# Kernel tuning notes

Hardware: AMD Instinct MI355X
Metric: run time of the kernel (lower is better)

## Reference

```python
import jax, jax.numpy as jnp
import numpy as np

B, N, F_NUM, H_NUM = 2, 8192, 64, 64


def _linear_params(key, fan_in, fan_out, bias=True):
    k1, k2 = jax.random.split(key)
    bound = 1.0 / np.sqrt(fan_in)
    W = jax.random.uniform(k1, (fan_in, fan_out), minval=-bound, maxval=bound, dtype=jnp.float32)
    if bias:
        b = jax.random.uniform(k2, (fan_out,), minval=-bound, maxval=bound, dtype=jnp.float32)
        return W, b
    return W


def setup_inputs() -> dict:
    key = jax.random.key(0)
    ks = jax.random.split(key, 12)
    Wk, bk = _linear_params(ks[0], F_NUM, H_NUM)
    Wa, ba = _linear_params(ks[1], H_NUM, F_NUM)
    Wq = _linear_params(ks[2], H_NUM, H_NUM, bias=False)
    Wks = _linear_params(ks[3], H_NUM, H_NUM, bias=False)
    Wv = _linear_params(ks[4], H_NUM, H_NUM, bias=False)
    Wp1, bp1 = _linear_params(ks[5], 4, H_NUM)
    Wp2, bp2 = _linear_params(ks[6], H_NUM, H_NUM)
    Wt1, bt1 = _linear_params(ks[7], H_NUM, H_NUM)
    Wt2, bt2 = _linear_params(ks[8], H_NUM, H_NUM)
    xyzp = jax.random.normal(ks[9], (B, N, 4), dtype=jnp.float32)
    features = jax.random.normal(ks[10], (B, N, F_NUM), dtype=jnp.float32)
    return dict(xyzp=xyzp, features=features, Wk=Wk, bk=bk, Wq=Wq, Wks=Wks, Wv=Wv,
                Wp1=Wp1, bp1=bp1, Wp2=Wp2, bp2=bp2, Wt1=Wt1, bt1=bt1, Wt2=Wt2, bt2=bt2,
                Wa=Wa, ba=ba, k_nearest=16)


def _knn_idx(xyz, K):
    sq = jnp.sum(xyz * xyz, axis=-1)                      # [B,N]
    d = sq[:, :, None] + sq[:, None, :] - 2.0 * jnp.einsum('bnd,bmd->bnm', xyz, xyz)
    _, idx = jax.lax.top_k(-d, K)                         # [B,N,K] nearest (incl. self)
    return idx


def _knn_gather(x, idx):
    # x: [B,N,C], idx: [B,N,K] -> [B,N,K,C]
    return jax.vmap(lambda xb, ib: xb[ib])(x, idx)


def reference(xyzp, features, Wk, bk, Wq, Wks, Wv, Wp1, bp1, Wp2, bp2,
              Wt1, bt1, Wt2, bt2, Wa, ba, k_nearest):
    xyz = xyzp[:, :, :3]
    idx = _knn_idx(xyz, k_nearest)                        # [B,N,K]
    # positional encoding MLP on relative xyzp
    rel = xyzp[:, :, None, :] - _knn_gather(xyzp, idx)    # [B,N,K,4]
    pos_enc = jax.nn.relu(rel @ Wp1 + bp1) @ Wp2 + bp2    # [B,N,K,H]
    x = features @ Wk + bk                                # [B,N,H]
    q = x @ Wq                                            # [B,N,H]
    k = _knn_gather(x @ Wks, idx)                         # [B,N,K,H]
    v = _knn_gather(x @ Wv, idx)                          # [B,N,K,H]
    a_in = q[:, :, None, :] - k + pos_enc                 # [B,N,K,H]
    attn = jax.nn.relu(a_in @ Wt1 + bt1) @ Wt2 + bt2      # [B,N,K,H]
    attn = jax.nn.softmax(attn / np.sqrt(H_NUM).astype(np.float32), axis=-2)
    res = jnp.einsum('bnkh,bnkh->bnh', attn, v + pos_enc) # per-channel weighted sum over K
    return res @ Wa + ba + features
```

## Files before the change

### kernel.cpp

```cpp
#include <hip/hip_runtime.h>

#define NPTS 8192
#define HDIM 64
#define KNN 16
#define LOG2E 1.4426950408889634f

typedef __attribute__((ext_vector_type(8))) short bf8_t;
typedef __attribute__((ext_vector_type(4))) float f4_t;
#define MFMA16(a, b, c) __builtin_amdgcn_mfma_f32_16x16x32_bf16(a, b, c, 0, 0, 0)

__device__ __forceinline__ float fast_exp(float x) {
    float y = x * LOG2E;
    float r;
    asm volatile("v_exp_f32 %0, %1\n\ts_nop 1" : "=v"(r) : "v"(y));
    return r;
}
__device__ __forceinline__ unsigned short f2b(float x) {
    unsigned v = __float_as_uint(x);
    return (unsigned short)((v + 0x7FFFu + ((v >> 16) & 1u)) >> 16);
}

#define OFF_QW   0u
#define OFF_KW   (4u << 20)
#define OFF_VW   (8u << 20)
#define OFF_FRAG (12u << 20)
#define OFF_KNN  ((12u << 20) + 32768u)

__global__ void prefrag_kernel(const float* __restrict__ Wp2,
                               const float* __restrict__ Wt1,
                               const float* __restrict__ Wt2,
                               unsigned short* __restrict__ dst)
{
    int i = blockIdx.x * 256 + threadIdx.x;
    if (i >= 3 * 4096) return;
    int st = i >> 12, e = i & 4095;
    const float* W = (st == 0) ? Wp2 : (st == 1) ? Wt1 : Wt2;
    int k = e >> 6, n = e & 63;
    int s = k >> 5, quad = (k >> 3) & 3, j = k & 7;
    int t = n >> 4, l = quad * 16 + (n & 15);
    dst[st * 4096 + (s * 4 + t) * 512 + l * 8 + j] = f2b(W[e]);
}

__global__ __launch_bounds__(1024) void proj_kernel(
    const float* __restrict__ feat,
    const float* __restrict__ Wk, const float* __restrict__ bk,
    const float* __restrict__ Wq, const float* __restrict__ Wks,
    const float* __restrict__ Wv,
    float* __restrict__ qw, float* __restrict__ kw, float* __restrict__ vw)
{
    __shared__ __align__(16) float4 sW[4][1024];
    int tid = threadIdx.x;
    sW[0][tid] = ((const float4*)Wk)[tid];
    sW[1][tid] = ((const float4*)Wq)[tid];
    sW[2][tid] = ((const float4*)Wks)[tid];
    sW[3][tid] = ((const float4*)Wv)[tid];
    __syncthreads();
    const float* sWk  = (const float*)sW[0];
    const float* sWq  = (const float*)sW[1];
    const float* sWks = (const float*)sW[2];
    const float* sWv  = (const float*)sW[3];

    int w = tid >> 6, lane = tid & 63;
    int p = blockIdx.x * 16 + w;
    float f = feat[(size_t)p * HDIM + lane];
    float x = bk[lane];
    #pragma unroll 8
    for (int c = 0; c < 64; ++c) x += __shfl(f, c) * sWk[c * 64 + lane];
    float q = 0.f, k = 0.f, v = 0.f;
    #pragma unroll 8
    for (int c = 0; c < 64; ++c) {
        float xc = __shfl(x, c);
        q += xc * sWq[c * 64 + lane];
        k += xc * sWks[c * 64 + lane];
        v += xc * sWv[c * 64 + lane];
    }
    qw[(size_t)p * HDIM + lane] = q;
    kw[(size_t)p * HDIM + lane] = k;
    vw[(size_t)p * HDIM + lane] = v;
}

__global__ __launch_bounds__(256) void knn4_kernel(
    const float* __restrict__ xyzp, int* __restrict__ knnIdx)
{
    int w = threadIdx.x >> 6, lane = threadIdx.x & 63;
    int wid = blockIdx.x * 4 + w;
    int pbase = wid * 4;
    int b = pbase >> 13;
    int nbase = pbase & (NPTS - 1);
    const float4* xb4 = (const float4*)xyzp + (size_t)b * NPTS;

    float qx[4], qy[4], qz[4], qs[4];
    #pragma unroll
    for (int qi = 0; qi < 4; ++qi) {
        float4 s = xb4[nbase + qi];
        qx[qi] = s.x; qy[qi] = s.y; qz[qi] = s.z;
        qs[qi] = s.x * s.x + s.y * s.y + s.z * s.z;
    }

    float dh[4][4]; int ih[4][4];
    #pragma unroll
    for (int qi = 0; qi < 4; ++qi)
        #pragma unroll
        for (int j = 0; j < 4; ++j) { dh[qi][j] = 3.4e38f; ih[qi][j] = 0x7fffffff; }

    for (int t = 0; t < NPTS / 256; ++t) {
        float4 c[4];
        #pragma unroll
        for (int u = 0; u < 4; ++u)
            c[u] = xb4[(t * 4 + u) * 64 + lane];
        #pragma unroll
        for (int u = 0; u < 4; ++u) {
            int m = (t * 4 + u) * 64 + lane;
            float cs = c[u].x * c[u].x + c[u].y * c[u].y + c[u].z * c[u].z;
            #pragma unroll
            for (int qi = 0; qi < 4; ++qi) {
                float d = qs[qi] + cs
                        - 2.0f * (qx[qi] * c[u].x + qy[qi] * c[u].y + qz[qi] * c[u].z);
                if (d < dh[qi][3]) {
                    dh[qi][3] = d; ih[qi][3] = m;
                    #pragma unroll
                    for (int j = 3; j >= 1; --j)
                        if (dh[qi][j] < dh[qi][j - 1]) {
                            float td = dh[qi][j]; dh[qi][j] = dh[qi][j - 1]; dh[qi][j - 1] = td;
                            int ti = ih[qi][j]; ih[qi][j] = ih[qi][j - 1]; ih[qi][j - 1] = ti;
                        }
                }
            }
        }
    }

    #pragma unroll
    for (int qi = 0; qi < 4; ++qi) {
        int mynb = 0, head = 0;
        #pragma unroll 1
        for (int r = 0; r < KNN; ++r) {
            float d = dh[qi][0]; int i = ih[qi][0];
            #pragma unroll
            for (int s = 1; s < 64; s <<= 1) {
                float d2 = __shfl_xor(d, s); int i2 = __shfl_xor(i, s);
                if (d2 < d || (d2 == d && i2 < i)) { d = d2; i = i2; }
            }
            if (lane == r) mynb = i;
            if (ih[qi][0] == i) {
                dh[qi][0] = dh[qi][1]; ih[qi][0] = ih[qi][1];
                dh[qi][1] = dh[qi][2]; ih[qi][1] = ih[qi][2];
                dh[qi][2] = dh[qi][3]; ih[qi][2] = ih[qi][3];
                dh[qi][3] = 3.4e38f; ih[qi][3] = 0x7fffffff;
                ++head;
            }
        }
        if (__any(head >= 4)) {
            float eh[16]; int ei[16];
            #pragma unroll
            for (int j = 0; j < 16; ++j) { eh[j] = 3.4e38f; ei[j] = 0x7fffffff; }
            for (int t = 0; t < NPTS / 64; ++t) {
                int m = t * 64 + lane;
                float4 c4 = xb4[m];
                float cs = c4.x * c4.x + c4.y * c4.y + c4.z * c4.z;
                float d = qs[qi] + cs
                        - 2.0f * (qx[qi] * c4.x + qy[qi] * c4.y + qz[qi] * c4.z);
                if (d < eh[15]) {
                    eh[15] = d; ei[15] = m;
                    #pragma unroll
                    for (int j = 15; j >= 1; --j)
                        if (eh[j] < eh[j - 1]) {
                            float td = eh[j]; eh[j] = eh[j - 1]; eh[j - 1] = td;
                            int ti = ei[j]; ei[j] = ei[j - 1]; ei[j - 1] = ti;
                        }
                }
            }
            #pragma unroll 1
            for (int r = 0; r < KNN; ++r) {
                float d = eh[0]; int i = ei[0];
                #pragma unroll
                for (int s = 1; s < 64; s <<= 1) {
                    float d2 = __shfl_xor(d, s); int i2 = __shfl_xor(i, s);
                    if (d2 < d || (d2 == d && i2 < i)) { d = d2; i = i2; }
                }
                if (lane == r) mynb = i;
                if (ei[0] == i) {
                    #pragma unroll
                    for (int j = 0; j < 15; ++j) { eh[j] = eh[j + 1]; ei[j] = ei[j + 1]; }
                    eh[15] = 3.4e38f; ei[15] = 0x7fffffff;
                }
            }
        }
        mynb = min(max(mynb, 0), NPTS - 1);
        if (lane < KNN) knnIdx[(size_t)(pbase + qi) * KNN + lane] = mynb;
    }
}

__global__ __launch_bounds__(256) void LocalTransformer_80513456931527_kernel(
    const float* __restrict__ xyzp, const float* __restrict__ features,
    const float* __restrict__ Wp1,  const float* __restrict__ bp1,
    const float* __restrict__ bp2,  const float* __restrict__ bt1,
    const float* __restrict__ bt2,
    const float* __restrict__ Wa,   const float* __restrict__ ba,
    const float* __restrict__ qw, const float* __restrict__ kw,
    const float* __restrict__ vw,
    const unsigned short* __restrict__ fragw,
    const int* __restrict__ knnIdx,
    float* __restrict__ out)
{
    __shared__ __align__(16) float sBounce[4][16 * 68 + 4];

    int tid = threadIdx.x, w = tid >> 6, lane = tid & 63;
    int p = blockIdx.x * 4 + w;
    int b = p >> 13;
    float* bb = sBounce[w];

    int quad = lane >> 4, l15 = lane & 15;
    int mynb = knnIdx[(size_t)p * KNN + l15];
    mynb = min(max(mynb, 0), NPTS - 1);
    int nb_a = mynb;
    int nbm[4];
    #pragma unroll
    for (int r = 0; r < 4; ++r) nbm[r] = __shfl(mynb, quad * 4 + r);

    const float4 xq4 = *(const float4*)(xyzp + (size_t)p * 4);
    const float4 xn4 = *(const float4*)(xyzp + ((size_t)b * NPTS + nb_a) * 4);
    float rel0 = xq4.x - xn4.x, rel1 = xq4.y - xn4.y;
    float rel2 = xq4.z - xn4.z, rel3 = xq4.w - xn4.w;

    bf8_t pe1f[2];
    #pragma unroll
    for (int s = 0; s < 2; ++s) {
        int hb = s * 32 + quad * 8;
        float W0[8], W1[8], W2[8], W3[8], Bb[8];
        *(float4*)&W0[0] = *(const float4*)(Wp1 +       hb);
        *(float4*)&W0[4] = *(const float4*)(Wp1 +       hb + 4);
        *(float4*)&W1[0] = *(const float4*)(Wp1 +  64 + hb);
        *(float4*)&W1[4] = *(const float4*)(Wp1 +  64 + hb + 4);
        *(float4*)&W2[0] = *(const float4*)(Wp1 + 128 + hb);
        *(float4*)&W2[4] = *(const float4*)(Wp1 + 128 + hb + 4);
        *(float4*)&W3[0] = *(const float4*)(Wp1 + 192 + hb);
        *(float4*)&W3[4] = *(const float4*)(Wp1 + 192 + hb + 4);
        *(float4*)&Bb[0] = *(const float4*)(bp1 + hb);
        *(float4*)&Bb[4] = *(const float4*)(bp1 + hb + 4);
        #pragma unroll
        for (int j = 0; j < 8; ++j) {
            float a = Bb[j] + rel0 * W0[j] + rel1 * W1[j]
                            + rel2 * W2[j] + rel3 * W3[j];
            pe1f[s][j] = (short)f2b(fmaxf(a, 0.f));
        }
    }

    const bf8_t* BW = (const bf8_t*)fragw;
    f4_t pe2c[4];
    #pragma unroll
    for (int t = 0; t < 4; ++t) {
        f4_t acc = {0.f, 0.f, 0.f, 0.f};
        acc = MFMA16(pe1f[0], BW[0 * 512 + (0 * 4 + t) * 64 + lane], acc);
        acc = MFMA16(pe1f[1], BW[0 * 512 + (1 * 4 + t) * 64 + lane], acc);
        float bias = bp2[t * 16 + l15];
        #pragma unroll
        for (int r = 0; r < 4; ++r) acc[r] += bias;
        pe2c[t] = acc;
    }

    f4_t ainc[4], vpec[4];
    #pragma unroll
    for (int t = 0; t < 4; ++t) {
        float qv = qw[(size_t)p * HDIM + t * 16 + l15];
        #pragma unroll
        for (int r = 0; r < 4; ++r) {
            size_t nbo = ((size_t)b * NPTS + nbm[r]) * HDIM + t * 16 + l15;
            ainc[t][r] = qv - kw[nbo] + pe2c[t][r];
            vpec[t][r] = vw[nbo] + pe2c[t][r];
        }
    }

    #pragma unroll
    for (int t = 0; t < 4; ++t)
        #pragma unroll
        for (int r = 0; r < 4; ++r)
            bb[(quad * 4 + r) * 68 + t * 16 + l15] = ainc[t][r];
    asm volatile("s_waitcnt lgkmcnt(0)" ::: "memory");
    bf8_t af[2];
    #pragma unroll
    for (int s = 0; s < 2; ++s) {
        float tmp[8];
        *(float4*)&tmp[0] = *(const float4*)&bb[l15 * 68 + s * 32 + quad * 8];
        *(float4*)&tmp[4] = *(const float4*)&bb[l15 * 68 + s * 32 + quad * 8 + 4];
        #pragma unroll
        for (int j = 0; j < 8; ++j) af[s][j] = (short)f2b(tmp[j]);
    }

    f4_t t1c[4];
    #pragma unroll
    for (int t = 0; t < 4; ++t) {
        f4_t acc = {0.f, 0.f, 0.f, 0.f};
        acc = MFMA16(af[0], BW[1 * 512 + (0 * 4 + t) * 64 + lane], acc);
        acc = MFMA16(af[1], BW[1 * 512 + (1 * 4 + t) * 64 + lane], acc);
        float bias = bt1[t * 16 + l15];
        #pragma unroll
        for (int r = 0; r < 4; ++r) t1c[t][r] = fmaxf(acc[r] + bias, 0.f);
    }

    asm volatile("s_waitcnt lgkmcnt(0)" ::: "memory");
    #pragma unroll
    for (int t = 0; t < 4; ++t)
        #pragma unroll
        for (int r = 0; r < 4; ++r)
            bb[(quad * 4 + r) * 68 + t * 16 + l15] = t1c[t][r];
    asm volatile("s_waitcnt lgkmcnt(0)" ::: "memory");
    bf8_t tf[2];
    #pragma unroll
    for (int s = 0; s < 2; ++s) {
        float tmp[8];
        *(float4*)&tmp[0] = *(const float4*)&bb[l15 * 68 + s * 32 + quad * 8];
        *(float4*)&tmp[4] = *(const float4*)&bb[l15 * 68 + s * 32 + quad * 8 + 4];
        #pragma unroll
        for (int j = 0; j < 8; ++j) tf[s][j] = (short)f2b(tmp[j]);
    }

    f4_t lgc[4];
    #pragma unroll
    for (int t = 0; t < 4; ++t) {
        f4_t acc = {0.f, 0.f, 0.f, 0.f};
        acc = MFMA16(tf[0], BW[2 * 512 + (0 * 4 + t) * 64 + lane], acc);
        acc = MFMA16(tf[1], BW[2 * 512 + (1 * 4 + t) * 64 + lane], acc);
        float bias = bt2[t * 16 + l15];
        #pragma unroll
        for (int r = 0; r < 4; ++r) lgc[t][r] = (acc[r] + bias) * 0.125f;
    }

    float res[4];
    #pragma unroll
    for (int t = 0; t < 4; ++t) {
        float m0 = fmaxf(fmaxf(lgc[t][0], lgc[t][1]), fmaxf(lgc[t][2], lgc[t][3]));
        m0 = fmaxf(m0, __shfl_xor(m0, 16));
        m0 = fmaxf(m0, __shfl_xor(m0, 32));
        float e0 = fast_exp(lgc[t][0] - m0), e1 = fast_exp(lgc[t][1] - m0);
        float e2 = fast_exp(lgc[t][2] - m0), e3 = fast_exp(lgc[t][3] - m0);
        float sl = e0 + e1 + e2 + e3;
        float rl = e0 * vpec[t][0] + e1 * vpec[t][1]
                 + e2 * vpec[t][2] + e3 * vpec[t][3];
        sl += __shfl_xor(sl, 16); sl += __shfl_xor(sl, 32);
        rl += __shfl_xor(rl, 16); rl += __shfl_xor(rl, 32);
        res[t] = rl / sl;
    }

    float rh = (quad == 0) ? res[0] : (quad == 1) ? res[1]
             : (quad == 2) ? res[2] : res[3];
    float f = features[(size_t)p * HDIM + lane];
    float o = ba[lane];
    #pragma unroll 8
    for (int c = 0; c < 64; ++c) o += __shfl(rh, c) * Wa[c * 64 + lane];
    out[(size_t)p * HDIM + lane] = o + f;
}

extern "C" void kernel_launch(void* const* d_in, const int* in_sizes, int n_in,
                              void* d_out, int out_size, void* d_ws, size_t ws_size,
                              hipStream_t stream)
{
    (void)in_sizes; (void)n_in; (void)out_size; (void)ws_size;
    const float* xyzp     = (const float*)d_in[0];
    const float* features = (const float*)d_in[1];
    const float* Wk  = (const float*)d_in[2];
    const float* bk  = (const float*)d_in[3];
    const float* Wq  = (const float*)d_in[4];
    const float* Wks = (const float*)d_in[5];
    const float* Wv  = (const float*)d_in[6];
    const float* Wp1 = (const float*)d_in[7];
    const float* bp1 = (const float*)d_in[8];
    const float* Wp2 = (const float*)d_in[9];
    const float* bp2 = (const float*)d_in[10];
    const float* Wt1 = (const float*)d_in[11];
    const float* bt1 = (const float*)d_in[12];
    const float* Wt2 = (const float*)d_in[13];
    const float* bt2 = (const float*)d_in[14];
    const float* Wa  = (const float*)d_in[15];
    const float* ba  = (const float*)d_in[16];
    float* out = (float*)d_out;
    char* ws = (char*)d_ws;

    float* qw = (float*)(ws + OFF_QW);
    float* kw = (float*)(ws + OFF_KW);
    float* vw = (float*)(ws + OFF_VW);
    unsigned short* fragw = (unsigned short*)(ws + OFF_FRAG);
    int* knnIdx = (int*)(ws + OFF_KNN);

    prefrag_kernel<<<48, 256, 0, stream>>>(Wp2, Wt1, Wt2, fragw);
    proj_kernel<<<(2 * NPTS) / 16, 1024, 0, stream>>>(
        features, Wk, bk, Wq, Wks, Wv, qw, kw, vw);
    knn4_kernel<<<(2 * NPTS) / 16, 256, 0, stream>>>(xyzp, knnIdx);
    LocalTransformer_80513456931527_kernel<<<(2 * NPTS) / 4, 256, 0, stream>>>(
        xyzp, features, Wp1, bp1, bp2, bt1, bt2, Wa, ba,
        qw, kw, vw, fragw, knnIdx, out);
}
```

Measured before the change: 375.0 us.

## Split rare KNN fallback path into a separate fix-up kernel

Moves the rare full-rescan fallback (used when one lane contributed four or more of a query's 16 neighbours) out of the main KNN kernel into a separate knnfix kernel, driven by per-wave failure flags written to the workspace. The main kernel no longer carries the 16-entry register heap, and launch_bounds(256,4) is added, so register pressure should drop and occupancy rise. The cost is one extra kernel launch, whose waves mostly exit early after reading a flag.

```diff
diff --git a/kernel.cpp b/kernel.cpp
--- a/kernel.cpp
+++ b/kernel.cpp
@@ -25,6 +25,7 @@
 #define OFF_VW   (8u << 20)
 #define OFF_FRAG (12u << 20)
 #define OFF_KNN  ((12u << 20) + 32768u)
+#define OFF_FLAG ((13u << 20) + 32768u)
 
 __global__ void prefrag_kernel(const float* __restrict__ Wp2,
                                const float* __restrict__ Wt1,
@@ -79,8 +80,9 @@
     vw[(size_t)p * HDIM + lane] = v;
 }
 
-__global__ __launch_bounds__(256) void knn4_kernel(
-    const float* __restrict__ xyzp, int* __restrict__ knnIdx)
+__global__ __launch_bounds__(256, 4) void knn4_kernel(
+    const float* __restrict__ xyzp, int* __restrict__ knnIdx,
+    int* __restrict__ flagw)
 {
     int w = threadIdx.x >> 6, lane = threadIdx.x & 63;
     int wid = blockIdx.x * 4 + w;
@@ -129,6 +131,7 @@
         }
     }
 
+    int failmask = 0;
     #pragma unroll
     for (int qi = 0; qi < 4; ++qi) {
         int mynb = 0, head = 0;
@@ -149,40 +152,64 @@
                 ++head;
             }
         }
-        if (__any(head >= 4)) {
-            float eh[16]; int ei[16];
+        if (__any(head >= 4)) failmask |= (1 << qi);
+        mynb = min(max(mynb, 0), NPTS - 1);
+        if (lane < KNN) knnIdx[(size_t)(pbase + qi) * KNN + lane] = mynb;
+    }
+    if (lane == 0) flagw[wid] = failmask;
+}
+
+__global__ __launch_bounds__(256) void knnfix_kernel(
+    const float* __restrict__ xyzp, const int* __restrict__ flagw,
+    int* __restrict__ knnIdx)
+{
+    int w = threadIdx.x >> 6, lane = threadIdx.x & 63;
+    int wid = blockIdx.x * 4 + w;
+    int failmask = flagw[wid];
+    if (failmask == 0) return;
+    int pbase = wid * 4;
+    int b = pbase >> 13;
+    int nbase = pbase & (NPTS - 1);
+    const float4* xb4 = (const float4*)xyzp + (size_t)b * NPTS;
+
+    #pragma unroll 1
+    for (int qi = 0; qi < 4; ++qi) {
+        if (!((failmask >> qi) & 1)) continue;
+        float4 s = xb4[nbase + qi];
+        float qx = s.x, qy = s.y, qz = s.z;
+        float qs = qx * qx + qy * qy + qz * qz;
+        float eh[16]; int ei[16];
+        #pragma unroll
+        for (int j = 0; j < 16; ++j) { eh[j] = 3.4e38f; ei[j] = 0x7fffffff; }
+        for (int t = 0; t < NPTS / 64; ++t) {
+            int m = t * 64 + lane;
+            float4 c4 = xb4[m];
+            float cs = c4.x * c4.x + c4.y * c4.y + c4.z * c4.z;
+            float d = qs + cs - 2.0f * (qx * c4.x + qy * c4.y + qz * c4.z);
+            if (d < eh[15]) {
+                eh[15] = d; ei[15] = m;
+                #pragma unroll
+                for (int j = 15; j >= 1; --j)
+                    if (eh[j] < eh[j - 1]) {
+                        float td = eh[j]; eh[j] = eh[j - 1]; eh[j - 1] = td;
+                        int ti = ei[j]; ei[j] = ei[j - 1]; ei[j - 1] = ti;
+                    }
+            }
+        }
+        int mynb = 0;
+        #pragma unroll 1
+        for (int r = 0; r < KNN; ++r) {
+            float d = eh[0]; int i = ei[0];
             #pragma unroll
-            for (int j = 0; j < 16; ++j) { eh[j] = 3.4e38f; ei[j] = 0x7fffffff; }
-            for (int t = 0; t < NPTS / 64; ++t) {
-                int m = t * 64 + lane;
-                float4 c4 = xb4[m];
-                float cs = c4.x * c4.x + c4.y * c4.y + c4.z * c4.z;
-                float d = qs[qi] + cs
-                        - 2.0f * (qx[qi] * c4.x + qy[qi] * c4.y + qz[qi] * c4.z);
-                if (d < eh[15]) {
-                    eh[15] = d; ei[15] = m;
-                    #pragma unroll
-                    for (int j = 15; j >= 1; --j)
-                        if (eh[j] < eh[j - 1]) {
-                            float td = eh[j]; eh[j] = eh[j - 1]; eh[j - 1] = td;
-                            int ti = ei[j]; ei[j] = ei[j - 1]; ei[j - 1] = ti;
-                        }
-                }
-            }
-            #pragma unroll 1
-            for (int r = 0; r < KNN; ++r) {
-                float d = eh[0]; int i = ei[0];
+            for (int s2 = 1; s2 < 64; s2 <<= 1) {
+                float d2 = __shfl_xor(d, s2); int i2 = __shfl_xor(i, s2);
+                if (d2 < d || (d2 == d && i2 < i)) { d = d2; i = i2; }
+            }
+            if (lane == r) mynb = i;
+            if (ei[0] == i) {
                 #pragma unroll
-                for (int s = 1; s < 64; s <<= 1) {
-                    float d2 = __shfl_xor(d, s); int i2 = __shfl_xor(i, s);
-                    if (d2 < d || (d2 == d && i2 < i)) { d = d2; i = i2; }
-                }
-                if (lane == r) mynb = i;
-                if (ei[0] == i) {
-                    #pragma unroll
-                    for (int j = 0; j < 15; ++j) { eh[j] = eh[j + 1]; ei[j] = ei[j + 1]; }
-                    eh[15] = 3.4e38f; ei[15] = 0x7fffffff;
-                }
+                for (int j = 0; j < 15; ++j) { eh[j] = eh[j + 1]; ei[j] = ei[j + 1]; }
+                eh[15] = 3.4e38f; ei[15] = 0x7fffffff;
             }
         }
         mynb = min(max(mynb, 0), NPTS - 1);
@@ -380,11 +407,13 @@
     float* vw = (float*)(ws + OFF_VW);
     unsigned short* fragw = (unsigned short*)(ws + OFF_FRAG);
     int* knnIdx = (int*)(ws + OFF_KNN);
+    int* flagw  = (int*)(ws + OFF_FLAG);
 
     prefrag_kernel<<<48, 256, 0, stream>>>(Wp2, Wt1, Wt2, fragw);
     proj_kernel<<<(2 * NPTS) / 16, 1024, 0, stream>>>(
         features, Wk, bk, Wq, Wks, Wv, qw, kw, vw);
-    knn4_kernel<<<(2 * NPTS) / 16, 256, 0, stream>>>(xyzp, knnIdx);
+    knn4_kernel<<<(2 * NPTS) / 16, 256, 0, stream>>>(xyzp, knnIdx, flagw);
+    knnfix_kernel<<<(2 * NPTS) / 16, 256, 0, stream>>>(xyzp, flagw, knnIdx);
     LocalTransformer_80513456931527_kernel<<<(2 * NPTS) / 4, 256, 0, stream>>>(
         xyzp, features, Wp1, bp1, bp2, bt1, bt2, Wa, ba,
         qw, kw, vw, fragw, knnIdx, out);
```

Measured after the change: 428.8 us. 14.4% more time.
